# Kernel optimization log

Measured on AMD Instinct MI355X. Metric: run time of the kernel, lower is better.

The kernel has to match this reference:

```python
import jax, jax.numpy as jnp
import numpy as np


def setup_inputs() -> dict:
    key = jax.random.key(0)
    ks = jax.random.split(key, 9)
    b, t_q, t_k, n_q, n_k = 4, 128, 512, 512, 512
    out_size = 512
    s = 0.02  # small init scale for weights
    return {
        "query": jax.random.normal(ks[0], (b, t_q, n_q), jnp.float32),
        "keys": jax.random.normal(ks[1], (b, t_k, n_k), jnp.float32),
        "values": jax.random.normal(ks[2], (b, t_k, n_k), jnp.float32),
        "W_q": jax.random.normal(ks[3], (n_k, n_q), jnp.float32) * s,
        "b_q": jnp.zeros((n_k,), jnp.float32),
        "w_att": jax.random.normal(ks[4], (n_k,), jnp.float32) * s,
        "b_att": jnp.zeros((1,), jnp.float32),
        "W_out": jax.random.normal(ks[5], (out_size, n_q + n_k), jnp.float32) * s,
        "b_out": jnp.zeros((out_size,), jnp.float32),
    }


def reference(query, keys, values, W_q, b_q, w_att, b_att, W_out, b_out):
    # linear_q: [b, t_q, query_size] -> [b, t_q, key_size]
    att_query = jnp.einsum("bqd,nd->bqn", query, W_q) + b_q
    # Bahdanau additive score: tanh(q + k) projected by linear_att (key_size -> 1)
    # intermediate: [b, t_q, t_k, n]
    sum_qk = jnp.tanh(att_query[:, :, None, :] + keys[:, None, :, :])
    scores = jnp.einsum("bqkn,n->bqk", sum_qk, w_att) + b_att[0]
    # mask is None by default; dropout p=0 -> identity
    probs = jax.nn.softmax(scores, axis=-1)  # [b, t_q, t_k]
    context = jnp.einsum("bqk,bkn->bqn", probs, values)
    # linear_out on concat([query, context]) + tanh nonlinearity
    cat = jnp.concatenate([query, context], axis=-1)
    out = jnp.tanh(jnp.einsum("bqc,oc->bqo", cat, W_out) + b_out)
    return out, probs
```

## Files before the change

### kernel.cpp

```cpp
#include <hip/hip_runtime.h>


#include <hip/hip_fp16.h>

#define BB    4
#define TQ    128
#define TK    512
#define NN    512
#define OUTSZ 512
#define CATSZ 1024
#define K2E   2.8853900817779268f
#define L2E   1.4426950408889634f
#define MAT   262144
#define WS_HALVES (11 * MAT)

typedef __attribute__((ext_vector_type(4))) _Float16 half4;

#if __has_builtin(__builtin_amdgcn_exp2f)
#define EXP2F(x) __builtin_amdgcn_exp2f(x)
#else
#define EXP2F(x) exp2f(x)
#endif
#if __has_builtin(__builtin_amdgcn_rcpf)
#define RCPF(x) __builtin_amdgcn_rcpf(x)
#else
#define RCPF(x) (1.0f / (x))
#endif

__device__ __forceinline__ float fast_tanh(float x) {
  float e = EXP2F(x * K2E);
  return fmaf(-2.0f, RCPF(e + 1.0f), 1.0f);
}
__device__ __forceinline__ float waveRedSum(float s) {
  #pragma unroll
  for (int m = 32; m >= 1; m >>= 1) s += __shfl_xor(s, m, 64);
  return s;
}
__device__ __forceinline__ float waveRedMax(float s) {
  #pragma unroll
  for (int m = 32; m >= 1; m >>= 1) s = fmaxf(s, __shfl_xor(s, m, 64));
  return s;
}
__device__ __forceinline__ float fma4(float4 w, float4 v, float acc) {
  acc = fmaf(w.x, v.x, acc); acc = fmaf(w.y, v.y, acc);
  acc = fmaf(w.z, v.z, acc); acc = fmaf(w.w, v.w, acc);
  return acc;
}
__device__ __forceinline__ float4 fma4sh(float4 a, half4 w, float s) {
  a.x = fmaf((float)w.x, s, a.x); a.y = fmaf((float)w.y, s, a.y);
  a.z = fmaf((float)w.z, s, a.z); a.w = fmaf((float)w.w, s, a.w);
  return a;
}
__device__ __forceinline__ float4 scqh(float4 s, half4 E, float A, float w) {
  s.x = fmaf(w, RCPF(fmaf((float)E.x, A, 1.0f)), s.x);
  s.y = fmaf(w, RCPF(fmaf((float)E.y, A, 1.0f)), s.y);
  s.z = fmaf(w, RCPF(fmaf((float)E.z, A, 1.0f)), s.z);
  s.w = fmaf(w, RCPF(fmaf((float)E.w, A, 1.0f)), s.w);
  return s;
}

__global__ __launch_bounds__(256)
void pack_kernel(const float* __restrict__ keys, const float* __restrict__ W_q,
                 const float* __restrict__ W_out, const float* __restrict__ values,
                 _Float16* __restrict__ ws)
{
  __shared__ float tile[32][33];
  const int idx = blockIdx.x;
  if (idx >= 1792) {
    int r = idx - 1792;
    size_t off = (size_t)r * 2048 + threadIdx.x * 8;
    float4 a = *(const float4*)(values + off);
    float4 b = *(const float4*)(values + off + 4);
    _Float16* dst = ws + (size_t)7 * MAT + off;
    half4 h0 = {(_Float16)a.x, (_Float16)a.y, (_Float16)a.z, (_Float16)a.w};
    half4 h1 = {(_Float16)b.x, (_Float16)b.y, (_Float16)b.z, (_Float16)b.w};
    *(half4*)(dst) = h0;
    *(half4*)(dst + 4) = h1;
    return;
  }
  const float* src; _Float16* dst; int M, N; float scale; int by, bx; bool doExp;
  if (idx < 1024) {
    int b = idx >> 8, r = idx & 255;
    by = r >> 4; bx = r & 15;
    src = keys + (size_t)b * MAT; dst = ws + (size_t)b * MAT;
    M = 512; N = 512; scale = K2E; doExp = true;
  } else if (idx < 1280) {
    int r = idx - 1024; by = r >> 4; bx = r & 15;
    src = W_q; dst = ws + (size_t)4 * MAT; M = 512; N = 512; scale = 1.0f; doExp = false;
  } else {
    int r = idx - 1280; by = r >> 5; bx = r & 31;
    src = W_out; dst = ws + (size_t)5 * MAT; M = 512; N = 1024; scale = 1.0f; doExp = false;
  }
  const int tx = threadIdx.x & 31, ty = threadIdx.x >> 5;
  #pragma unroll
  for (int i = 0; i < 32; i += 8)
    tile[ty + i][tx] = src[(size_t)(by * 32 + ty + i) * N + bx * 32 + tx] * scale;
  __syncthreads();
  #pragma unroll
  for (int i = 0; i < 32; i += 8) {
    float v = tile[tx][ty + i];
    if (doExp) v = EXP2F(v);
    dst[(size_t)(bx * 32 + ty + i) * M + by * 32 + tx] = (_Float16)v;
  }
}

__global__ __launch_bounds__(1024, 4)
void attn_main(const float* __restrict__ query,
               const float* __restrict__ b_q, const float* __restrict__ w_att,
               const float* __restrict__ b_att, const float* __restrict__ b_out,
               const _Float16* __restrict__ ws,
               float* __restrict__ out, float* __restrict__ probs)
{
  __shared__ __align__(16) float2 catI[CATSZ];
  __shared__ __align__(16) float4 paw[NN];
  __shared__ __align__(16) float2 prI[TK];
  __shared__ __align__(16) float  pt[8][2][NN];
  __shared__ float redm[2][8], reds2[2][8], redw[8];

  const _Float16* wsKeys = ws;
  const _Float16* wsWq   = ws + (size_t)4 * MAT;
  const _Float16* wsWout = ws + (size_t)5 * MAT;
  const _Float16* wsVal  = ws + (size_t)7 * MAT;

  const int t    = threadIdx.x;
  const int qh   = t >> 9;
  const int u    = t & 511;
  const int G    = t >> 7;
  const int v    = t & 127;
  const int wave = t >> 6, lane = t & 63, wq8 = wave & 7;

  const int p  = blockIdx.x;
  const int b  = (p & 7) >> 1;
  const int qg = ((p >> 3) << 1) | (p & 1);
  const int qabs0 = qg * 2;

  const float batt = b_att[0];

  float w_own = 0.f;
  if (qh == 0) {
    float q0 = query[((size_t)(b * TQ + qabs0 + 0)) * NN + u];
    float q1 = query[((size_t)(b * TQ + qabs0 + 1)) * NN + u];
    catI[u] = make_float2(q0, q1);
  } else {
    w_own = w_att[u];
  }
  if (qh == 1) {
    float wp = waveRedSum(w_own);
    if (lane == 0) redw[wq8] = wp;
  }
  __syncthreads();
  const float sumW = redw[0]+redw[1]+redw[2]+redw[3]+redw[4]+redw[5]+redw[6]+redw[7];

  {
    const _Float16* wq = wsWq + 4 * v;
    float4 a0 = {0,0,0,0}, a1 = {0,0,0,0};
    #pragma unroll 4
    for (int j = 0; j < 64; j += 2) {
      int d = 64 * G + j;
      half4 wA = *(const half4*)(wq + (size_t)d * 512);
      half4 wB = *(const half4*)(wq + (size_t)(d + 1) * 512);
      float4 qq = *(const float4*)(&catI[d]);
      a0 = fma4sh(a0, wA, qq.x); a1 = fma4sh(a1, wA, qq.y);
      a0 = fma4sh(a0, wB, qq.z); a1 = fma4sh(a1, wB, qq.w);
    }
    *(float4*)(&pt[G][0][4 * v]) = a0;
    *(float4*)(&pt[G][1][4 * v]) = a1;
  }
  __syncthreads();
  {
    float s = pt[0][qh][u] + pt[1][qh][u] + pt[2][qh][u] + pt[3][qh][u]
            + pt[4][qh][u] + pt[5][qh][u] + pt[6][qh][u] + pt[7][qh][u];
    float A = EXP2F(K2E * (s + b_q[u]));
    if (qh == 0) { paw[u].x = A; paw[u].z = w_att[u]; }
    else         { paw[u].y = A; }
  }
  __syncthreads();

  {
    const _Float16* ke = wsKeys + (size_t)b * MAT + 4 * v;
    float4 s0 = {0,0,0,0}, s1 = {0,0,0,0};
    #pragma unroll 4
    for (int j = 0; j < 64; ++j) {
      int n = 64 * G + j;
      half4 E   = *(const half4*)(ke + (size_t)n * 512);
      float4 pw = paw[n];
      s0 = scqh(s0, E, pw.x, pw.z);
      s1 = scqh(s1, E, pw.y, pw.z);
    }
    *(float4*)(&pt[G][0][4 * v]) = s0;
    *(float4*)(&pt[G][1][4 * v]) = s1;
  }
  __syncthreads();

  {
    float s = pt[0][qh][u] + pt[1][qh][u] + pt[2][qh][u] + pt[3][qh][u]
            + pt[4][qh][u] + pt[5][qh][u] + pt[6][qh][u] + pt[7][qh][u];
    float sc = batt + sumW - 2.0f * s;
    float m = waveRedMax(sc);
    if (lane == 0) redm[qh][wq8] = m;
    __syncthreads();
    float bm = fmaxf(fmaxf(fmaxf(redm[qh][0],redm[qh][1]),fmaxf(redm[qh][2],redm[qh][3])),
                     fmaxf(fmaxf(redm[qh][4],redm[qh][5]),fmaxf(redm[qh][6],redm[qh][7])));
    float e = EXP2F((sc - bm) * L2E);
    float se = waveRedSum(e);
    if (lane == 0) reds2[qh][wq8] = se;
    __syncthreads();
    float bs = reds2[qh][0]+reds2[qh][1]+reds2[qh][2]+reds2[qh][3]
             + reds2[qh][4]+reds2[qh][5]+reds2[qh][6]+reds2[qh][7];
    float pv = e * RCPF(bs);
    if (qh == 0) prI[u].x = pv; else prI[u].y = pv;
    probs[((size_t)(b * TQ + qabs0 + qh)) * TK + u] = pv;
  }
  __syncthreads();

  {
    const _Float16* vv = wsVal + ((size_t)(b * TK + 64 * G)) * NN + 4 * v;
    float4 c0 = {0,0,0,0}, c1 = {0,0,0,0};
    #pragma unroll 4
    for (int j = 0; j < 64; j += 2) {
      half4 vA = *(const half4*)(vv + (size_t)j * NN);
      half4 vB = *(const half4*)(vv + (size_t)(j + 1) * NN);
      float4 pp = *(const float4*)(&prI[64 * G + j]);
      c0 = fma4sh(c0, vA, pp.x); c1 = fma4sh(c1, vA, pp.y);
      c0 = fma4sh(c0, vB, pp.z); c1 = fma4sh(c1, vB, pp.w);
    }
    *(float4*)(&pt[G][0][4 * v]) = c0;
    *(float4*)(&pt[G][1][4 * v]) = c1;
  }
  __syncthreads();
  {
    float s = pt[0][qh][u] + pt[1][qh][u] + pt[2][qh][u] + pt[3][qh][u]
            + pt[4][qh][u] + pt[5][qh][u] + pt[6][qh][u] + pt[7][qh][u];
    if (qh == 0) catI[512 + u].x = s; else catI[512 + u].y = s;
  }
  __syncthreads();

  {
    const _Float16* wo = wsWout + 4 * v;
    float4 o0 = {0,0,0,0}, o1 = {0,0,0,0};
    #pragma unroll 4
    for (int j = 0; j < 128; j += 2) {
      int c = 128 * G + j;
      half4 wA = *(const half4*)(wo + (size_t)c * 512);
      half4 wB = *(const half4*)(wo + (size_t)(c + 1) * 512);
      float4 cc = *(const float4*)(&catI[c]);
      o0 = fma4sh(o0, wA, cc.x); o1 = fma4sh(o1, wA, cc.y);
      o0 = fma4sh(o0, wB, cc.z); o1 = fma4sh(o1, wB, cc.w);
    }
    *(float4*)(&pt[G][0][4 * v]) = o0;
    *(float4*)(&pt[G][1][4 * v]) = o1;
  }
  __syncthreads();
  {
    float s = pt[0][qh][u] + pt[1][qh][u] + pt[2][qh][u] + pt[3][qh][u]
            + pt[4][qh][u] + pt[5][qh][u] + pt[6][qh][u] + pt[7][qh][u];
    float oo = s + b_out[u];
    out[((size_t)(b * TQ + qabs0 + qh)) * OUTSZ + u] = fast_tanh(oo);
  }
}

__device__ __forceinline__ float sc4f(float4 w, float4 k, float4 a, float acc) {
  acc = fmaf(w.x, RCPF(EXP2F(fmaf(k.x, K2E, a.x)) + 1.0f), acc);
  acc = fmaf(w.y, RCPF(EXP2F(fmaf(k.y, K2E, a.y)) + 1.0f), acc);
  acc = fmaf(w.z, RCPF(EXP2F(fmaf(k.z, K2E, a.z)) + 1.0f), acc);
  acc = fmaf(w.w, RCPF(EXP2F(fmaf(k.w, K2E, a.w)) + 1.0f), acc);
  return acc;
}

__global__ __launch_bounds__(1024, 4)
void attn_fallback(const float* __restrict__ query, const float* __restrict__ keys,
                   const float* __restrict__ values, const float* __restrict__ W_q,
                   const float* __restrict__ b_q, const float* __restrict__ w_att,
                   const float* __restrict__ b_att, const float* __restrict__ W_out,
                   const float* __restrict__ b_out,
                   float* __restrict__ out, float* __restrict__ probs)
{
  __shared__ __align__(16) float qv[2][NN];
  __shared__ __align__(16) float aqc[2][NN];
  __shared__ __align__(16) float wv[NN];
  __shared__ __align__(16) float pr[2][TK];
  __shared__ __align__(16) float ctx[2][NN];
  __shared__ __align__(16) float part[2][2][NN];
  __shared__ float redm[2][8], reds[2][8], redw[8];

  const int t = threadIdx.x, H = t >> 9, u = t & 511;
  const int wave = t >> 6, lane = t & 63, wq8 = wave & 7;
  const int p = blockIdx.x, b = (p & 7) >> 1;
  const int qg = ((p >> 3) << 1) | (p & 1), qabs0 = qg * 2;
  const float batt = b_att[0];

  if (H == 0) wv[u] = w_att[u];
  qv[H][u] = query[((size_t)(b * TQ + qabs0 + H)) * NN + u];
  __syncthreads();
  if (H == 0) {
    float wp = waveRedSum(wv[u]);
    if (lane == 0) redw[wq8] = wp;
  }
  __syncthreads();
  const float sumW = redw[0]+redw[1]+redw[2]+redw[3]+redw[4]+redw[5]+redw[6]+redw[7];

  {
    const float4* wq4 = (const float4*)(W_q + (size_t)u * NN + 256 * H);
    const float4* x4  = (const float4*)(qv[0] + 256 * H);
    const float4* y4  = (const float4*)(qv[1] + 256 * H);
    float a0=0.f, a0b=0.f, a1=0.f, a1b=0.f;
    #pragma unroll 2
    for (int c = 0; c < 16; ++c) {
      float4 wA=wq4[4*c+0], wB=wq4[4*c+1], wC=wq4[4*c+2], wD=wq4[4*c+3];
      float4 xA=x4[4*c+0], xB=x4[4*c+1], xC=x4[4*c+2], xD=x4[4*c+3];
      a0 = fma4(wA,xA,a0); a0b = fma4(wB,xB,a0b);
      a0 = fma4(wC,xC,a0); a0b = fma4(wD,xD,a0b);
      float4 yA=y4[4*c+0], yB=y4[4*c+1], yC=y4[4*c+2], yD=y4[4*c+3];
      a1 = fma4(wA,yA,a1); a1b = fma4(wB,yB,a1b);
      a1 = fma4(wC,yC,a1); a1b = fma4(wD,yD,a1b);
    }
    part[H][0][u] = a0 + a0b; part[H][1][u] = a1 + a1b;
  }
  __syncthreads();
  aqc[H][u] = (part[0][H][u] + part[1][H][u] + b_q[u]) * K2E;
  __syncthreads();

  {
    const float4* kr  = (const float4*)(keys + ((size_t)(b * TK) + u) * NN + 256 * H);
    const float4* a0p = (const float4*)(aqc[0] + 256 * H);
    const float4* a1p = (const float4*)(aqc[1] + 256 * H);
    const float4* w4  = (const float4*)(wv + 256 * H);
    float s0 = 0.f, s1 = 0.f;
    #pragma unroll 2
    for (int c = 0; c < 16; ++c) {
      float4 kA=kr[4*c+0], kB=kr[4*c+1], kC=kr[4*c+2], kD=kr[4*c+3];
      float4 wA=w4[4*c+0], wB=w4[4*c+1], wC=w4[4*c+2], wD=w4[4*c+3];
      float4 aA=a0p[4*c+0], aB=a0p[4*c+1], aC=a0p[4*c+2], aD=a0p[4*c+3];
      s0 = sc4f(wA,kA,aA,s0); s0 = sc4f(wB,kB,aB,s0);
      s0 = sc4f(wC,kC,aC,s0); s0 = sc4f(wD,kD,aD,s0);
      float4 bA=a1p[4*c+0], bB=a1p[4*c+1], bC=a1p[4*c+2], bD=a1p[4*c+3];
      s1 = sc4f(wA,kA,bA,s1); s1 = sc4f(wB,kB,bB,s1);
      s1 = sc4f(wC,kC,bC,s1); s1 = sc4f(wD,kD,bD,s1);
    }
    part[H][0][u] = s0; part[H][1][u] = s1;
  }
  __syncthreads();

  {
    float sc = batt + sumW - 2.0f * (part[0][H][u] + part[1][H][u]);
    float m = waveRedMax(sc);
    if (lane == 0) redm[H][wq8] = m;
    __syncthreads();
    float bm = fmaxf(fmaxf(fmaxf(redm[H][0],redm[H][1]),fmaxf(redm[H][2],redm[H][3])),
                     fmaxf(fmaxf(redm[H][4],redm[H][5]),fmaxf(redm[H][6],redm[H][7])));
    float e = EXP2F((sc - bm) * L2E);
    float se = waveRedSum(e);
    if (lane == 0) reds[H][wq8] = se;
    __syncthreads();
    float bs = reds[H][0]+reds[H][1]+reds[H][2]+reds[H][3]
             + reds[H][4]+reds[H][5]+reds[H][6]+reds[H][7];
    float pv = e * RCPF(bs);
    pr[H][u] = pv;
    probs[((size_t)(b * TQ + qabs0 + H)) * TK + u] = pv;
  }
  __syncthreads();

  {
    const float* vcol = values + ((size_t)(b * TK) + 256 * H) * NN + u;
    const float4* p0 = (const float4*)(pr[0] + 256 * H);
    const float4* p1 = (const float4*)(pr[1] + 256 * H);
    float c0a=0.f, c0b=0.f, c1a=0.f, c1b=0.f;
    #pragma unroll 2
    for (int k = 0; k < 256; k += 8) {
      float v0 = vcol[(size_t)(k+0)*NN]; float v1 = vcol[(size_t)(k+1)*NN];
      float v2 = vcol[(size_t)(k+2)*NN]; float v3 = vcol[(size_t)(k+3)*NN];
      float v4 = vcol[(size_t)(k+4)*NN]; float v5 = vcol[(size_t)(k+5)*NN];
      float v6 = vcol[(size_t)(k+6)*NN]; float v7 = vcol[(size_t)(k+7)*NN];
      float4 pA = p0[k>>2], pB = p0[(k>>2)+1];
      float4 qA = p1[k>>2], qB = p1[(k>>2)+1];
      c0a = fmaf(pA.x,v0,c0a); c0a = fmaf(pA.y,v1,c0a);
      c0b = fmaf(pA.z,v2,c0b); c0b = fmaf(pA.w,v3,c0b);
      c0a = fmaf(pB.x,v4,c0a); c0a = fmaf(pB.y,v5,c0a);
      c0b = fmaf(pB.z,v6,c0b); c0b = fmaf(pB.w,v7,c0b);
      c1a = fmaf(qA.x,v0,c1a); c1a = fmaf(qA.y,v1,c1a);
      c1b = fmaf(qA.z,v2,c1b); c1b = fmaf(qA.w,v3,c1b);
      c1a = fmaf(qB.x,v4,c1a); c1a = fmaf(qB.y,v5,c1a);
      c1b = fmaf(qB.z,v6,c1b); c1b = fmaf(qB.w,v7,c1b);
    }
    part[H][0][u] = c0a + c0b; part[H][1][u] = c1a + c1b;
  }
  __syncthreads();
  ctx[H][u] = part[0][H][u] + part[1][H][u];
  __syncthreads();

  {
    const float4* wo = (const float4*)(W_out + (size_t)u * CATSZ + 512 * H);
    const float4* x4 = (H == 0) ? (const float4*)qv[0] : (const float4*)ctx[0];
    const float4* y4 = (H == 0) ? (const float4*)qv[1] : (const float4*)ctx[1];
    float o0=0.f, o0b=0.f, o1=0.f, o1b=0.f;
    #pragma unroll 2
    for (int c = 0; c < 32; ++c) {
      float4 wA=wo[4*c+0], wB=wo[4*c+1], wC=wo[4*c+2], wD=wo[4*c+3];
      float4 xA=x4[4*c+0], xB=x4[4*c+1], xC=x4[4*c+2], xD=x4[4*c+3];
      o0 = fma4(wA,xA,o0); o0b = fma4(wB,xB,o0b);
      o0 = fma4(wC,xC,o0); o0b = fma4(wD,xD,o0b);
      float4 yA=y4[4*c+0], yB=y4[4*c+1], yC=y4[4*c+2], yD=y4[4*c+3];
      o1 = fma4(wA,yA,o1); o1b = fma4(wB,yB,o1b);
      o1 = fma4(wC,yC,o1); o1b = fma4(wD,yD,o1b);
    }
    part[H][0][u] = o0 + o0b; part[H][1][u] = o1 + o1b;
  }
  __syncthreads();
  {
    float oo = part[0][H][u] + part[1][H][u] + b_out[u];
    out[((size_t)(b * TQ + qabs0 + H)) * OUTSZ + u] = fast_tanh(oo);
  }
}

extern "C" void kernel_launch(void* const* d_in, const int* in_sizes, int n_in,
                              void* d_out, int out_size, void* d_ws, size_t ws_size,
                              hipStream_t stream) {
  const float* query = (const float*)d_in[0];
  const float* keys  = (const float*)d_in[1];
  const float* vals  = (const float*)d_in[2];
  const float* W_q   = (const float*)d_in[3];
  const float* b_q   = (const float*)d_in[4];
  const float* w_att = (const float*)d_in[5];
  const float* b_att = (const float*)d_in[6];
  const float* W_out = (const float*)d_in[7];
  const float* b_out = (const float*)d_in[8];

  float* out   = (float*)d_out;
  float* probs = out + (size_t)BB * TQ * OUTSZ;

  if (ws_size >= (size_t)WS_HALVES * sizeof(_Float16)) {
    _Float16* ws = (_Float16*)d_ws;
    pack_kernel<<<dim3(2304), dim3(256), 0, stream>>>(keys, W_q, W_out, vals, ws);
    attn_main<<<dim3(BB * TQ / 2), dim3(1024), 0, stream>>>(
        query, b_q, w_att, b_att, b_out, ws, out, probs);
  } else {
    attn_fallback<<<dim3(BB * TQ / 2), dim3(1024), 0, stream>>>(
        query, keys, vals, W_q, b_q, w_att, b_att, W_out, b_out, out, probs);
  }
}
```

Before: 130.2 us.

## Use packed fp16 dot2 for projection, context and output GEMVs with pair-interleaved packing

The pack kernel now stores W_q, W_out and values in a pair-interleaved fp16 layout, so each 16-byte load holds two reduction rows for four output columns. The main kernel keeps the query/context concat and the probabilities in fp16 shared buffers. The three GEMV-like stages use v_dot2 fp16 instructions, which halves the FMA count and the instruction overhead. The trade-off is that activations are now quantised to fp16 too, which lowers accuracy, and the values pack uses more, smaller blocks. The keys-loop unroll factor is also raised.

New measurement: 117.3 us. 1.11x faster.

```diff
diff --git a/kernel.cpp b/kernel.cpp
--- a/kernel.cpp
+++ b/kernel.cpp
@@ -1,7 +1,6 @@
 #include <hip/hip_runtime.h>
-
-
 #include <hip/hip_fp16.h>
+
 
 #define BB    4
 #define TQ    128
@@ -15,6 +14,7 @@
 #define WS_HALVES (11 * MAT)
 
 typedef __attribute__((ext_vector_type(4))) _Float16 half4;
+typedef __attribute__((ext_vector_type(2))) _Float16 h2;
 
 #if __has_builtin(__builtin_amdgcn_exp2f)
 #define EXP2F(x) __builtin_amdgcn_exp2f(x)
@@ -27,6 +27,19 @@
 #define RCPF(x) (1.0f / (x))
 #endif
 
+__device__ __forceinline__ h2 u2h(unsigned int u) {
+  union { unsigned int i; h2 h; } v; v.i = u; return v.h;
+}
+#if __has_builtin(__builtin_amdgcn_fdot2)
+__device__ __forceinline__ float FDOT2(h2 a, h2 b, float c) {
+  return __builtin_amdgcn_fdot2(a, b, c, false);
+}
+#else
+__device__ __forceinline__ float FDOT2(h2 a, h2 b, float c) {
+  return fmaf((float)a.x, (float)b.x, fmaf((float)a.y, (float)b.y, c));
+}
+#endif
+
 __device__ __forceinline__ float fast_tanh(float x) {
   float e = EXP2F(x * K2E);
   return fmaf(-2.0f, RCPF(e + 1.0f), 1.0f);
@@ -45,11 +58,6 @@
   acc = fmaf(w.x, v.x, acc); acc = fmaf(w.y, v.y, acc);
   acc = fmaf(w.z, v.z, acc); acc = fmaf(w.w, v.w, acc);
   return acc;
-}
-__device__ __forceinline__ float4 fma4sh(float4 a, half4 w, float s) {
-  a.x = fmaf((float)w.x, s, a.x); a.y = fmaf((float)w.y, s, a.y);
-  a.z = fmaf((float)w.z, s, a.z); a.w = fmaf((float)w.w, s, a.w);
-  return a;
 }
 __device__ __forceinline__ float4 scqh(float4 s, half4 E, float A, float w) {
   s.x = fmaf(w, RCPF(fmaf((float)E.x, A, 1.0f)), s.x);
@@ -57,6 +65,13 @@
   s.z = fmaf(w, RCPF(fmaf((float)E.z, A, 1.0f)), s.z);
   s.w = fmaf(w, RCPF(fmaf((float)E.w, A, 1.0f)), s.w);
   return s;
+}
+__device__ __forceinline__ void dotq(float4& r0, float4& r1, uint4 wp, uint2 cp) {
+  h2 c0 = u2h(cp.x), c1 = u2h(cp.y);
+  r0.x = FDOT2(u2h(wp.x), c0, r0.x); r1.x = FDOT2(u2h(wp.x), c1, r1.x);
+  r0.y = FDOT2(u2h(wp.y), c0, r0.y); r1.y = FDOT2(u2h(wp.y), c1, r1.y);
+  r0.z = FDOT2(u2h(wp.z), c0, r0.z); r1.z = FDOT2(u2h(wp.z), c1, r1.z);
+  r0.w = FDOT2(u2h(wp.w), c0, r0.w); r1.w = FDOT2(u2h(wp.w), c1, r1.w);
 }
 
 __global__ __launch_bounds__(256)
@@ -66,41 +81,54 @@
 {
   __shared__ float tile[32][33];
   const int idx = blockIdx.x;
+  const int tx = threadIdx.x & 31, ty = threadIdx.x >> 5;
+
   if (idx >= 1792) {
     int r = idx - 1792;
-    size_t off = (size_t)r * 2048 + threadIdx.x * 8;
-    float4 a = *(const float4*)(values + off);
-    float4 b = *(const float4*)(values + off + 4);
-    _Float16* dst = ws + (size_t)7 * MAT + off;
-    half4 h0 = {(_Float16)a.x, (_Float16)a.y, (_Float16)a.z, (_Float16)a.w};
-    half4 h1 = {(_Float16)b.x, (_Float16)b.y, (_Float16)b.z, (_Float16)b.w};
-    *(half4*)(dst) = h0;
-    *(half4*)(dst + 4) = h1;
+    int b = r >> 8, k2 = r & 255;
+    const float* r0 = values + ((size_t)b * 512 + 2 * k2) * 512;
+    const float* r1 = r0 + 512;
+    int n0 = threadIdx.x * 2;
+    float2 a = *(const float2*)(r0 + n0);
+    float2 c = *(const float2*)(r1 + n0);
+    _Float16* dst = ws + (size_t)7 * MAT + (size_t)b * MAT + k2 * 1024 + n0 * 2;
+    half4 h = {(_Float16)a.x, (_Float16)c.x, (_Float16)a.y, (_Float16)c.y};
+    *(half4*)dst = h;
     return;
   }
-  const float* src; _Float16* dst; int M, N; float scale; int by, bx; bool doExp;
+
   if (idx < 1024) {
     int b = idx >> 8, r = idx & 255;
-    by = r >> 4; bx = r & 15;
-    src = keys + (size_t)b * MAT; dst = ws + (size_t)b * MAT;
-    M = 512; N = 512; scale = K2E; doExp = true;
-  } else if (idx < 1280) {
+    int by = r >> 4, bx = r & 15;
+    const float* src = keys + (size_t)b * MAT;
+    _Float16* dst = ws + (size_t)b * MAT;
+    #pragma unroll
+    for (int i = 0; i < 32; i += 8)
+      tile[ty + i][tx] = src[(size_t)(by * 32 + ty + i) * 512 + bx * 32 + tx] * K2E;
+    __syncthreads();
+    #pragma unroll
+    for (int i = 0; i < 32; i += 8)
+      dst[(size_t)(bx * 32 + ty + i) * 512 + by * 32 + tx] = (_Float16)EXP2F(tile[tx][ty + i]);
+    return;
+  }
+
+  const float* src; _Float16* dst; int N; int by, bx;
+  if (idx < 1280) {
     int r = idx - 1024; by = r >> 4; bx = r & 15;
-    src = W_q; dst = ws + (size_t)4 * MAT; M = 512; N = 512; scale = 1.0f; doExp = false;
+    src = W_q; dst = ws + (size_t)4 * MAT; N = 512;
   } else {
     int r = idx - 1280; by = r >> 5; bx = r & 31;
-    src = W_out; dst = ws + (size_t)5 * MAT; M = 512; N = 1024; scale = 1.0f; doExp = false;
-  }
-  const int tx = threadIdx.x & 31, ty = threadIdx.x >> 5;
+    src = W_out; dst = ws + (size_t)5 * MAT; N = 1024;
+  }
   #pragma unroll
   for (int i = 0; i < 32; i += 8)
-    tile[ty + i][tx] = src[(size_t)(by * 32 + ty + i) * N + bx * 32 + tx] * scale;
+    tile[ty + i][tx] = src[(size_t)(by * 32 + ty + i) * N + bx * 32 + tx];
   __syncthreads();
   #pragma unroll
   for (int i = 0; i < 32; i += 8) {
-    float v = tile[tx][ty + i];
-    if (doExp) v = EXP2F(v);
-    dst[(size_t)(bx * 32 + ty + i) * M + by * 32 + tx] = (_Float16)v;
+    int d = bx * 32 + ty + i;
+    int o = by * 32 + tx;
+    dst[(size_t)(d >> 1) * 1024 + o * 2 + (d & 1)] = (_Float16)tile[tx][ty + i];
   }
 }
 
@@ -111,16 +139,16 @@
                const _Float16* __restrict__ ws,
                float* __restrict__ out, float* __restrict__ probs)
 {
-  __shared__ __align__(16) float2 catI[CATSZ];
+  __shared__ __align__(16) _Float16 catH[2048];
   __shared__ __align__(16) float4 paw[NN];
-  __shared__ __align__(16) float2 prI[TK];
+  __shared__ __align__(16) _Float16 prH[1024];
   __shared__ __align__(16) float  pt[8][2][NN];
   __shared__ float redm[2][8], reds2[2][8], redw[8];
 
-  const _Float16* wsKeys = ws;
-  const _Float16* wsWq   = ws + (size_t)4 * MAT;
-  const _Float16* wsWout = ws + (size_t)5 * MAT;
-  const _Float16* wsVal  = ws + (size_t)7 * MAT;
+  const _Float16* wsKeys  = ws;
+  const _Float16* wsWqP   = ws + (size_t)4 * MAT;
+  const _Float16* wsWoutP = ws + (size_t)5 * MAT;
+  const _Float16* wsValP  = ws + (size_t)7 * MAT;
 
   const int t    = threadIdx.x;
   const int qh   = t >> 9;
@@ -140,7 +168,8 @@
   if (qh == 0) {
     float q0 = query[((size_t)(b * TQ + qabs0 + 0)) * NN + u];
     float q1 = query[((size_t)(b * TQ + qabs0 + 1)) * NN + u];
-    catI[u] = make_float2(q0, q1);
+    catH[(u >> 1) * 4 + (u & 1)]     = (_Float16)q0;
+    catH[(u >> 1) * 4 + 2 + (u & 1)] = (_Float16)q1;
   } else {
     w_own = w_att[u];
   }
@@ -152,16 +181,14 @@
   const float sumW = redw[0]+redw[1]+redw[2]+redw[3]+redw[4]+redw[5]+redw[6]+redw[7];
 
   {
-    const _Float16* wq = wsWq + 4 * v;
+    const _Float16* wq = wsWqP + 8 * v;
     float4 a0 = {0,0,0,0}, a1 = {0,0,0,0};
     #pragma unroll 4
-    for (int j = 0; j < 64; j += 2) {
-      int d = 64 * G + j;
-      half4 wA = *(const half4*)(wq + (size_t)d * 512);
-      half4 wB = *(const half4*)(wq + (size_t)(d + 1) * 512);
-      float4 qq = *(const float4*)(&catI[d]);
-      a0 = fma4sh(a0, wA, qq.x); a1 = fma4sh(a1, wA, qq.y);
-      a0 = fma4sh(a0, wB, qq.z); a1 = fma4sh(a1, wB, qq.w);
+    for (int j2 = 0; j2 < 32; ++j2) {
+      int d2 = 32 * G + j2;
+      uint4 wp = *(const uint4*)(wq + (size_t)d2 * 1024);
+      uint2 cp = *(const uint2*)(&catH[d2 * 4]);
+      dotq(a0, a1, wp, cp);
     }
     *(float4*)(&pt[G][0][4 * v]) = a0;
     *(float4*)(&pt[G][1][4 * v]) = a1;
@@ -179,7 +206,7 @@
   {
     const _Float16* ke = wsKeys + (size_t)b * MAT + 4 * v;
     float4 s0 = {0,0,0,0}, s1 = {0,0,0,0};
-    #pragma unroll 4
+    #pragma unroll 8
     for (int j = 0; j < 64; ++j) {
       int n = 64 * G + j;
       half4 E   = *(const half4*)(ke + (size_t)n * 512);
@@ -208,21 +235,20 @@
     float bs = reds2[qh][0]+reds2[qh][1]+reds2[qh][2]+reds2[qh][3]
              + reds2[qh][4]+reds2[qh][5]+reds2[qh][6]+reds2[qh][7];
     float pv = e * RCPF(bs);
-    if (qh == 0) prI[u].x = pv; else prI[u].y = pv;
+    prH[(u >> 1) * 4 + qh * 2 + (u & 1)] = (_Float16)pv;
     probs[((size_t)(b * TQ + qabs0 + qh)) * TK + u] = pv;
   }
   __syncthreads();
 
   {
-    const _Float16* vv = wsVal + ((size_t)(b * TK + 64 * G)) * NN + 4 * v;
+    const _Float16* vp = wsValP + (size_t)b * MAT + 8 * v;
     float4 c0 = {0,0,0,0}, c1 = {0,0,0,0};
     #pragma unroll 4
-    for (int j = 0; j < 64; j += 2) {
-      half4 vA = *(const half4*)(vv + (size_t)j * NN);
-      half4 vB = *(const half4*)(vv + (size_t)(j + 1) * NN);
-      float4 pp = *(const float4*)(&prI[64 * G + j]);
-      c0 = fma4sh(c0, vA, pp.x); c1 = fma4sh(c1, vA, pp.y);
-      c0 = fma4sh(c0, vB, pp.z); c1 = fma4sh(c1, vB, pp.w);
+    for (int j2 = 0; j2 < 32; ++j2) {
+      int k2 = 32 * G + j2;
+      uint4 vk = *(const uint4*)(vp + (size_t)k2 * 1024);
+      uint2 pp = *(const uint2*)(&prH[k2 * 4]);
+      dotq(c0, c1, vk, pp);
     }
     *(float4*)(&pt[G][0][4 * v]) = c0;
     *(float4*)(&pt[G][1][4 * v]) = c1;
@@ -231,21 +257,19 @@
   {
     float s = pt[0][qh][u] + pt[1][qh][u] + pt[2][qh][u] + pt[3][qh][u]
             + pt[4][qh][u] + pt[5][qh][u] + pt[6][qh][u] + pt[7][qh][u];
-    if (qh == 0) catI[512 + u].x = s; else catI[512 + u].y = s;
-  }
-  __syncthreads();
-
-  {
-    const _Float16* wo = wsWout + 4 * v;
+    catH[(256 + (u >> 1)) * 4 + qh * 2 + (u & 1)] = (_Float16)s;
+  }
+  __syncthreads();
+
+  {
+    const _Float16* wo = wsWoutP + 8 * v;
     float4 o0 = {0,0,0,0}, o1 = {0,0,0,0};
     #pragma unroll 4
-    for (int j = 0; j < 128; j += 2) {
-      int c = 128 * G + j;
-      half4 wA = *(const half4*)(wo + (size_t)c * 512);
-      half4 wB = *(const half4*)(wo + (size_t)(c + 1) * 512);
-      float4 cc = *(const float4*)(&catI[c]);
-      o0 = fma4sh(o0, wA, cc.x); o1 = fma4sh(o1, wA, cc.y);
-      o0 = fma4sh(o0, wB, cc.z); o1 = fma4sh(o1, wB, cc.w);
+    for (int j2 = 0; j2 < 64; ++j2) {
+      int c2 = 64 * G + j2;
+      uint4 wp = *(const uint4*)(wo + (size_t)c2 * 1024);
+      uint2 cp = *(const uint2*)(&catH[c2 * 4]);
+      dotq(o0, o1, wp, cp);
     }
     *(float4*)(&pt[G][0][4 * v]) = o0;
     *(float4*)(&pt[G][1][4 * v]) = o1;
@@ -430,7 +454,7 @@
 
   if (ws_size >= (size_t)WS_HALVES * sizeof(_Float16)) {
     _Float16* ws = (_Float16*)d_ws;
-    pack_kernel<<<dim3(2304), dim3(256), 0, stream>>>(keys, W_q, W_out, vals, ws);
+    pack_kernel<<<dim3(2816), dim3(256), 0, stream>>>(keys, W_q, W_out, vals, ws);
     attn_main<<<dim3(BB * TQ / 2), dim3(1024), 0, stream>>>(
         query, b_q, w_att, b_att, b_out, ws, out, probs);
   } else {
```
